# Performance work log

Measured on AMD Instinct MI355X. Metric: run time of the kernel, lower is better.

Reference implementation:

```python
import jax, jax.numpy as jnp
import numpy as np

# pywt db4 decomposition filters (dec_lo, dec_hi), length 8
DB4_DEC_LO = np.array([-0.010597401784997278, 0.032883011666982945,
                       0.030841381835986965, -0.18703481171888114,
                       -0.02798376941698385, 0.6308807679295904,
                       0.7148465705525415, 0.23037781330885523], dtype=np.float32)
DB4_DEC_HI = np.array([-0.23037781330885523, 0.7148465705525415,
                       -0.6308807679295904, -0.02798376941698385,
                       0.18703481171888114, 0.030841381835986965,
                       -0.032883011666982945, -0.010597401784997278], dtype=np.float32)
LEVEL = 3


def setup_inputs() -> dict:
    key = jax.random.key(0)
    x = jax.random.normal(key, (64, 32, 4096), dtype=jnp.float32)  # (B, N, T)
    return {"x": x,
            "dec_lo": jnp.asarray(DB4_DEC_LO),
            "dec_hi": jnp.asarray(DB4_DEC_HI)}


def _swt(x, dec_lo, dec_hi, level=LEVEL):
    """Stationary (a trous) wavelet transform, matching ptwt.swt semantics."""
    B, N, T = x.shape
    filt_len = dec_lo.shape[0]
    # ptwt flips the filters so conv1d (correlation) performs true convolution
    filt = jnp.stack([dec_lo[::-1], dec_hi[::-1]], axis=0)[:, None, :]  # (2, 1, L)
    res_lo = x.reshape(B * N, 1, T)
    details = []
    for lvl in range(level):
        dil = 2 ** lvl
        padl = dil * (filt_len // 2 - 1)
        padr = dil * (filt_len // 2)
        padded = jnp.pad(res_lo, ((0, 0), (0, 0), (padl, padr)), mode="wrap")  # circular
        res = jax.lax.conv_general_dilated(
            padded, filt, window_strides=(1,), padding="VALID",
            rhs_dilation=(dil,), dimension_numbers=("NCH", "OIH", "NCH"))  # (BN, 2, T)
        res_lo = res[:, 0:1, :]
        details.append(res[:, 1, :])
    # ptwt ordering: [cA_level, cD_level, ..., cD_1]
    coeffs = [res_lo[:, 0, :]] + details[::-1]
    stacked = jnp.stack(coeffs, axis=1)  # (B*N, level+1, T)
    return stacked.reshape(B, N, level + 1, T).transpose(0, 1, 3, 2)  # (B, N, T, level+1)


def reference(x, dec_lo, dec_hi):
    return _swt(x, dec_lo, dec_hi)
```

## Files before the change

### kernel.cpp

```cpp
#include <hip/hip_runtime.h>

#define TLEN 4096
#define NTHREADS 512
#define PER (TLEN / NTHREADS)

typedef float f32x4 __attribute__((ext_vector_type(4)));

__global__ __launch_bounds__(NTHREADS) void swt_db4_l3_kernel(
    const float* __restrict__ x,
    const float* __restrict__ lo_g,
    const float* __restrict__ hi_g,
    float* __restrict__ out)
{
    __shared__ float bufA[TLEN];
    __shared__ float bufB[TLEN];

    const int row = blockIdx.x;
    const int tid = threadIdx.x;

    float lo[8], hi[8];
#pragma unroll
    for (int j = 0; j < 8; ++j) { lo[j] = lo_g[j]; hi[j] = hi_g[j]; }

    const float* xr = x + (size_t)row * TLEN;

#pragma unroll
    for (int k = 0; k < PER / 4; ++k) {
        int idx = (tid + k * NTHREADS) * 4;
        f32x4 v = *reinterpret_cast<const f32x4*>(xr + idx);
        *reinterpret_cast<f32x4*>(&bufA[idx]) = v;
    }
    __syncthreads();

    float D1[PER], D2[PER], D3[PER], A3[PER];

#pragma unroll
    for (int k = 0; k < PER; ++k) {
        int t = tid + k * NTHREADS;
        float a = 0.f, d = 0.f;
#pragma unroll
        for (int j = 0; j < 8; ++j) {
            float v = bufA[(t + (4 - j)) & (TLEN - 1)];
            a = fmaf(lo[j], v, a);
            d = fmaf(hi[j], v, d);
        }
        D1[k] = d;
        bufB[t] = a;
    }
    __syncthreads();

#pragma unroll
    for (int k = 0; k < PER; ++k) {
        int t = tid + k * NTHREADS;
        float a = 0.f, d = 0.f;
#pragma unroll
        for (int j = 0; j < 8; ++j) {
            float v = bufB[(t + (4 - j) * 2) & (TLEN - 1)];
            a = fmaf(lo[j], v, a);
            d = fmaf(hi[j], v, d);
        }
        D2[k] = d;
        bufA[t] = a;
    }
    __syncthreads();

#pragma unroll
    for (int k = 0; k < PER; ++k) {
        int t = tid + k * NTHREADS;
        float a = 0.f, d = 0.f;
#pragma unroll
        for (int j = 0; j < 8; ++j) {
            float v = bufA[(t + (4 - j) * 4) & (TLEN - 1)];
            a = fmaf(lo[j], v, a);
            d = fmaf(hi[j], v, d);
        }
        D3[k] = d;
        A3[k] = a;
    }

    f32x4* outr = reinterpret_cast<f32x4*>(out + (size_t)row * TLEN * 4);
#pragma unroll
    for (int k = 0; k < PER; ++k) {
        int t = tid + k * NTHREADS;
        f32x4 v;
        v.x = A3[k]; v.y = D3[k]; v.z = D2[k]; v.w = D1[k];
        outr[t] = v;
    }
}

extern "C" void kernel_launch(void* const* d_in, const int* in_sizes, int n_in,
                              void* d_out, int out_size, void* d_ws, size_t ws_size,
                              hipStream_t stream) {
    const float* x  = (const float*)d_in[0];
    const float* lo = (const float*)d_in[1];
    const float* hi = (const float*)d_in[2];
    float* out = (float*)d_out;

    const int rows = 64 * 32;
    swt_db4_l3_kernel<<<dim3(rows), dim3(NTHREADS), 0, stream>>>(x, lo, hi, out);
}
```

Baseline: 38.21 us.

## Compute four contiguous outputs per thread with vectorized LDS window loads

Measured after the change: 52.07 us. 1.36x slower.

```diff
diff --git a/kernel.cpp b/kernel.cpp
--- a/kernel.cpp
+++ b/kernel.cpp
@@ -1,12 +1,17 @@
 #include <hip/hip_runtime.h>
 
 #define TLEN 4096
-#define NTHREADS 512
-#define PER (TLEN / NTHREADS)
+#define NT 256
+#define NGRP (TLEN / 4)
+#define GPT (NGRP / NT)
 
 typedef float f32x4 __attribute__((ext_vector_type(4)));
 
-__global__ __launch_bounds__(NTHREADS) void swt_db4_l3_kernel(
+__device__ __forceinline__ f32x4 ldv4(const float* p) {
+    return *reinterpret_cast<const f32x4*>(p);
+}
+
+__global__ __launch_bounds__(NT, 5) void swt_db4_l3_kernel(
     const float* __restrict__ x,
     const float* __restrict__ lo_g,
     const float* __restrict__ hi_g,
@@ -25,66 +30,122 @@
     const float* xr = x + (size_t)row * TLEN;
 
 #pragma unroll
-    for (int k = 0; k < PER / 4; ++k) {
-        int idx = (tid + k * NTHREADS) * 4;
-        f32x4 v = *reinterpret_cast<const f32x4*>(xr + idx);
-        *reinterpret_cast<f32x4*>(&bufA[idx]) = v;
+    for (int k = 0; k < 4; ++k) {
+        int idx = (tid + k * NT) * 4;
+        *reinterpret_cast<f32x4*>(&bufA[idx]) = ldv4(xr + idx);
     }
     __syncthreads();
 
-    float D1[PER], D2[PER], D3[PER], A3[PER];
+    float D1[GPT][4], D2[GPT][4];
 
 #pragma unroll
-    for (int k = 0; k < PER; ++k) {
-        int t = tid + k * NTHREADS;
-        float a = 0.f, d = 0.f;
+    for (int k = 0; k < GPT; ++k) {
+        int g = tid + k * NT;
+        float a[4] = {0,0,0,0}, d[4] = {0,0,0,0};
+        if (g >= 1 && g <= 1021) {
+            float w[16];
 #pragma unroll
-        for (int j = 0; j < 8; ++j) {
-            float v = bufA[(t + (4 - j)) & (TLEN - 1)];
-            a = fmaf(lo[j], v, a);
-            d = fmaf(hi[j], v, d);
+            for (int m = 0; m < 4; ++m)
+                *reinterpret_cast<f32x4*>(&w[4*m]) = ldv4(&bufA[4*g - 4 + 4*m]);
+#pragma unroll
+            for (int j = 0; j < 8; ++j)
+#pragma unroll
+                for (int i = 0; i < 4; ++i) {
+                    float v = w[i + 8 - j];
+                    a[i] = fmaf(lo[j], v, a[i]);
+                    d[i] = fmaf(hi[j], v, d[i]);
+                }
+        } else {
+#pragma unroll
+            for (int i = 0; i < 4; ++i) {
+                int t = 4*g + i;
+#pragma unroll
+                for (int j = 0; j < 8; ++j) {
+                    float v = bufA[(t + (4 - j)) & (TLEN - 1)];
+                    a[i] = fmaf(lo[j], v, a[i]);
+                    d[i] = fmaf(hi[j], v, d[i]);
+                }
+            }
         }
-        D1[k] = d;
-        bufB[t] = a;
+        f32x4 av; av.x = a[0]; av.y = a[1]; av.z = a[2]; av.w = a[3];
+        *reinterpret_cast<f32x4*>(&bufB[4*g]) = av;
+#pragma unroll
+        for (int i = 0; i < 4; ++i) D1[k][i] = d[i];
     }
     __syncthreads();
 
 #pragma unroll
-    for (int k = 0; k < PER; ++k) {
-        int t = tid + k * NTHREADS;
-        float a = 0.f, d = 0.f;
+    for (int k = 0; k < GPT; ++k) {
+        int g = tid + k * NT;
+        float a[4] = {0,0,0,0}, d[4] = {0,0,0,0};
+        if (g >= 2 && g <= 1021) {
+            float w[20];
 #pragma unroll
-        for (int j = 0; j < 8; ++j) {
-            float v = bufB[(t + (4 - j) * 2) & (TLEN - 1)];
-            a = fmaf(lo[j], v, a);
-            d = fmaf(hi[j], v, d);
+            for (int m = 0; m < 5; ++m)
+                *reinterpret_cast<f32x4*>(&w[4*m]) = ldv4(&bufB[4*g - 8 + 4*m]);
+#pragma unroll
+            for (int j = 0; j < 8; ++j)
+#pragma unroll
+                for (int i = 0; i < 4; ++i) {
+                    float v = w[i + 16 - 2*j];
+                    a[i] = fmaf(lo[j], v, a[i]);
+                    d[i] = fmaf(hi[j], v, d[i]);
+                }
+        } else {
+#pragma unroll
+            for (int i = 0; i < 4; ++i) {
+                int t = 4*g + i;
+#pragma unroll
+                for (int j = 0; j < 8; ++j) {
+                    float v = bufB[(t + (4 - j) * 2) & (TLEN - 1)];
+                    a[i] = fmaf(lo[j], v, a[i]);
+                    d[i] = fmaf(hi[j], v, d[i]);
+                }
+            }
         }
-        D2[k] = d;
-        bufA[t] = a;
+        f32x4 av; av.x = a[0]; av.y = a[1]; av.z = a[2]; av.w = a[3];
+        *reinterpret_cast<f32x4*>(&bufA[4*g]) = av;
+#pragma unroll
+        for (int i = 0; i < 4; ++i) D2[k][i] = d[i];
     }
     __syncthreads();
 
-#pragma unroll
-    for (int k = 0; k < PER; ++k) {
-        int t = tid + k * NTHREADS;
-        float a = 0.f, d = 0.f;
-#pragma unroll
-        for (int j = 0; j < 8; ++j) {
-            float v = bufA[(t + (4 - j) * 4) & (TLEN - 1)];
-            a = fmaf(lo[j], v, a);
-            d = fmaf(hi[j], v, d);
-        }
-        D3[k] = d;
-        A3[k] = a;
-    }
-
     f32x4* outr = reinterpret_cast<f32x4*>(out + (size_t)row * TLEN * 4);
 #pragma unroll
-    for (int k = 0; k < PER; ++k) {
-        int t = tid + k * NTHREADS;
-        f32x4 v;
-        v.x = A3[k]; v.y = D3[k]; v.z = D2[k]; v.w = D1[k];
-        outr[t] = v;
+    for (int k = 0; k < GPT; ++k) {
+        int g = tid + k * NT;
+        float a[4] = {0,0,0,0}, d[4] = {0,0,0,0};
+        if (g >= 3 && g <= 1019) {
+            float w[32];
+#pragma unroll
+            for (int m = 0; m < 8; ++m)
+                *reinterpret_cast<f32x4*>(&w[4*m]) = ldv4(&bufA[4*g - 12 + 4*m]);
+#pragma unroll
+            for (int j = 0; j < 8; ++j)
+#pragma unroll
+                for (int i = 0; i < 4; ++i) {
+                    float v = w[i + 28 - 4*j];
+                    a[i] = fmaf(lo[j], v, a[i]);
+                    d[i] = fmaf(hi[j], v, d[i]);
+                }
+        } else {
+#pragma unroll
+            for (int i = 0; i < 4; ++i) {
+                int t = 4*g + i;
+#pragma unroll
+                for (int j = 0; j < 8; ++j) {
+                    float v = bufA[(t + (4 - j) * 4) & (TLEN - 1)];
+                    a[i] = fmaf(lo[j], v, a[i]);
+                    d[i] = fmaf(hi[j], v, d[i]);
+                }
+            }
+        }
+#pragma unroll
+        for (int i = 0; i < 4; ++i) {
+            f32x4 v;
+            v.x = a[i]; v.y = d[i]; v.z = D2[k][i]; v.w = D1[k][i];
+            outr[4*g + i] = v;
+        }
     }
 }
 
@@ -97,5 +158,5 @@
     float* out = (float*)d_out;
 
     const int rows = 64 * 32;
-    swt_db4_l3_kernel<<<dim3(rows), dim3(NTHREADS), 0, stream>>>(x, lo, hi, out);
+    swt_db4_l3_kernel<<<dim3(rows), dim3(NT), 0, stream>>>(x, lo, hi, out);
 }
```

## Pad shared buffers with circular halos and use packed FMA for lo/hi

Applied to the files above, without the earlier changes.

Result: faster. 32.77 us (-14.3%).

```diff
diff --git a/kernel.cpp b/kernel.cpp
--- a/kernel.cpp
+++ b/kernel.cpp
@@ -1,90 +1,105 @@
 #include <hip/hip_runtime.h>
 
 #define TLEN 4096
-#define NTHREADS 512
-#define PER (TLEN / NTHREADS)
+#define NT 256
+#define PER 16
+#define SH 12
+#define RH 16
+#define BUFLEN (SH + TLEN + RH)
 
 typedef float f32x4 __attribute__((ext_vector_type(4)));
+typedef float f32x2 __attribute__((ext_vector_type(2)));
 
-__global__ __launch_bounds__(NTHREADS) void swt_db4_l3_kernel(
+__device__ __forceinline__ f32x4 ldv4(const float* p) {
+    return *reinterpret_cast<const f32x4*>(p);
+}
+
+__global__ __launch_bounds__(NT, 4) void swt_db4_l3_kernel(
     const float* __restrict__ x,
     const float* __restrict__ lo_g,
     const float* __restrict__ hi_g,
     float* __restrict__ out)
 {
-    __shared__ float bufA[TLEN];
-    __shared__ float bufB[TLEN];
+    __shared__ float bufA[BUFLEN];
+    __shared__ float bufB[BUFLEN];
 
     const int row = blockIdx.x;
     const int tid = threadIdx.x;
 
-    float lo[8], hi[8];
+    f32x2 c[8];
 #pragma unroll
-    for (int j = 0; j < 8; ++j) { lo[j] = lo_g[j]; hi[j] = hi_g[j]; }
+    for (int j = 0; j < 8; ++j) { c[j].x = lo_g[j]; c[j].y = hi_g[j]; }
 
     const float* xr = x + (size_t)row * TLEN;
 
 #pragma unroll
-    for (int k = 0; k < PER / 4; ++k) {
-        int idx = (tid + k * NTHREADS) * 4;
-        f32x4 v = *reinterpret_cast<const f32x4*>(xr + idx);
-        *reinterpret_cast<f32x4*>(&bufA[idx]) = v;
+    for (int k = 0; k < 4; ++k) {
+        int idx = (tid + k * NT) * 4;
+        f32x4 v = ldv4(xr + idx);
+        *reinterpret_cast<f32x4*>(&bufA[SH + idx]) = v;
+        if (k == 0 && tid < 4)
+            *reinterpret_cast<f32x4*>(&bufA[SH + TLEN + idx]) = v;
+        if (k == 3 && idx >= TLEN - SH)
+            *reinterpret_cast<f32x4*>(&bufA[idx - (TLEN - SH)]) = v;
     }
     __syncthreads();
 
-    float D1[PER], D2[PER], D3[PER], A3[PER];
+    float D1[PER], D2[PER];
 
 #pragma unroll
     for (int k = 0; k < PER; ++k) {
-        int t = tid + k * NTHREADS;
-        float a = 0.f, d = 0.f;
+        int t = tid + k * NT;
+        const float* s = &bufA[t + SH];
+        f32x2 acc; acc.x = 0.f; acc.y = 0.f;
 #pragma unroll
         for (int j = 0; j < 8; ++j) {
-            float v = bufA[(t + (4 - j)) & (TLEN - 1)];
-            a = fmaf(lo[j], v, a);
-            d = fmaf(hi[j], v, d);
+            float v = s[(4 - j)];
+            f32x2 vv; vv.x = v; vv.y = v;
+            acc = __builtin_elementwise_fma(c[j], vv, acc);
         }
-        D1[k] = d;
-        bufB[t] = a;
+        bufB[t + SH] = acc.x;
+        if (k == 0 && tid < RH)           bufB[t + SH + TLEN] = acc.x;
+        if (k == PER - 1 && t >= TLEN - SH) bufB[t + SH - TLEN] = acc.x;
+        D1[k] = acc.y;
     }
     __syncthreads();
 
 #pragma unroll
     for (int k = 0; k < PER; ++k) {
-        int t = tid + k * NTHREADS;
-        float a = 0.f, d = 0.f;
+        int t = tid + k * NT;
+        const float* s = &bufB[t + SH];
+        f32x2 acc; acc.x = 0.f; acc.y = 0.f;
 #pragma unroll
         for (int j = 0; j < 8; ++j) {
-            float v = bufB[(t + (4 - j) * 2) & (TLEN - 1)];
-            a = fmaf(lo[j], v, a);
-            d = fmaf(hi[j], v, d);
+            float v = s[(4 - j) * 2];
+            f32x2 vv; vv.x = v; vv.y = v;
+            acc = __builtin_elementwise_fma(c[j], vv, acc);
         }
-        D2[k] = d;
-        bufA[t] = a;
+        bufA[t + SH] = acc.x;
+        if (k == 0 && tid < RH)           bufA[t + SH + TLEN] = acc.x;
+        if (k == PER - 1 && t >= TLEN - SH) bufA[t + SH - TLEN] = acc.x;
+        D2[k] = acc.y;
     }
     __syncthreads();
-
-#pragma unroll
-    for (int k = 0; k < PER; ++k) {
-        int t = tid + k * NTHREADS;
-        float a = 0.f, d = 0.f;
-#pragma unroll
-        for (int j = 0; j < 8; ++j) {
-            float v = bufA[(t + (4 - j) * 4) & (TLEN - 1)];
-            a = fmaf(lo[j], v, a);
-            d = fmaf(hi[j], v, d);
-        }
-        D3[k] = d;
-        A3[k] = a;
-    }
 
     f32x4* outr = reinterpret_cast<f32x4*>(out + (size_t)row * TLEN * 4);
 #pragma unroll
     for (int k = 0; k < PER; ++k) {
-        int t = tid + k * NTHREADS;
-        f32x4 v;
-        v.x = A3[k]; v.y = D3[k]; v.z = D2[k]; v.w = D1[k];
-        outr[t] = v;
+        int t = tid + k * NT;
+        const float* s = &bufA[t + SH];
+        f32x2 acc; acc.x = 0.f; acc.y = 0.f;
+#pragma unroll
+        for (int j = 0; j < 8; ++j) {
+            float v = s[(4 - j) * 4];
+            f32x2 vv; vv.x = v; vv.y = v;
+            acc = __builtin_elementwise_fma(c[j], vv, acc);
+        }
+        f32x4 o;
+        o.x = acc.x;
+        o.y = acc.y;
+        o.z = D2[k];
+        o.w = D1[k];
+        outr[t] = o;
     }
 }
 
@@ -97,5 +112,5 @@
     float* out = (float*)d_out;
 
     const int rows = 64 * 32;
-    swt_db4_l3_kernel<<<dim3(rows), dim3(NTHREADS), 0, stream>>>(x, lo, hi, out);
+    swt_db4_l3_kernel<<<dim3(rows), dim3(NT), 0, stream>>>(x, lo, hi, out);
 }
```
